# Optimization experiments

Measured on AMD Instinct MI355X. Metric: run time of the kernel, lower is better.

Reference implementation:

```python
import jax, jax.numpy as jnp
import numpy as np
from jax import lax

DN = ('NCHW', 'OIHW', 'NCHW')

def _conv(x, k, stride):
    return lax.conv_general_dilated(x, k, (stride, stride), 'VALID', dimension_numbers=DN)

def setup_inputs() -> dict:
    key = jax.random.key(0)
    ks = jax.random.split(key, 20)
    B, E, A, D = 2048, 8, 6, 64 * 7 * 7  # batch, rm_states, actions, flat conv dim (3136)
    s = 0.05
    inp = {
        'state': jax.random.normal(ks[0], (B, 84, 84, 3), jnp.float32),
        'rm_state': jax.random.randint(ks[1], (B,), 0, E, jnp.int64),
        # conv encoder params
        'k1': jax.random.normal(ks[2], (32, 3, 8, 8), jnp.float32) * s,
        'c1': jnp.zeros((32,), jnp.float32),
        'k2': jax.random.normal(ks[3], (64, 32, 4, 4), jnp.float32) * s,
        'c2': jnp.zeros((64,), jnp.float32),
        'k3': jax.random.normal(ks[4], (64, 64, 3, 3), jnp.float32) * s,
        'c3': jnp.zeros((64,), jnp.float32),
        # stacked per-rm-state expert MLP params (E experts)
        'W1': jax.random.normal(ks[5], (E, D, 64), jnp.float32) * s,
        'B1': jnp.zeros((E, 64), jnp.float32),
        'W2': jax.random.normal(ks[6], (E, 64, 64), jnp.float32) * s,
        'B2': jnp.zeros((E, 64), jnp.float32),
        'W3': jax.random.normal(ks[7], (E, 64, 64), jnp.float32) * s,
        'B3': jnp.zeros((E, 64), jnp.float32),
        'W4': jax.random.normal(ks[8], (E, 64, 64), jnp.float32) * s,
        'B4': jnp.zeros((E, 64), jnp.float32),
        'W5': jax.random.normal(ks[9], (E, 64, 64), jnp.float32) * s,
        'B5': jnp.zeros((E, 64), jnp.float32),
        'W6': jax.random.normal(ks[10], (E, 64, A), jnp.float32) * s,
        'B6': jnp.zeros((E, A), jnp.float32),
    }
    return inp

def reference(state, rm_state, k1, c1, k2, c2, k3, c3,
              W1, B1, W2, B2, W3, B3, W4, B4, W5, B5, W6, B6):
    # NHWC -> NCHW (matches torch's view-based channel-first rearrangement intent)
    x = jnp.transpose(state, (0, 3, 1, 2))
    x = jax.nn.relu(_conv(x, k1, 4) + c1[None, :, None, None])
    x = jax.nn.relu(_conv(x, k2, 2) + c2[None, :, None, None])
    x = jax.nn.relu(_conv(x, k3, 1) + c3[None, :, None, None])
    B = x.shape[0]
    flat = x.reshape(B, -1)                              # [B, 3136]
    # batched expert MLPs: compute all experts, then gather per-sample expert output
    h = jax.nn.relu(jnp.einsum('bd,edh->ebh', flat, W1) + B1[:, None, :])  # [E,B,64]
    for W, Bb in ((W2, B2), (W3, B3), (W4, B4), (W5, B5)):
        h = jax.nn.relu(jnp.einsum('ebh,ehk->ebk', h, W) + Bb[:, None, :])
    out = jnp.einsum('ebh,eha->eba', h, W6) + B6[:, None, :]               # [E,B,A]
    return out[rm_state, jnp.arange(B)]                  # [B, A]
```

## Files before the change

kernel.cpp:

```cpp
#include <hip/hip_runtime.h>

#define BATCH 2048

typedef unsigned short u16;
typedef __attribute__((ext_vector_type(8))) short bf16x8;
typedef __attribute__((ext_vector_type(4))) float f32x4;

static __device__ __forceinline__ float b2f(u16 h) {
  union { unsigned u; float f; } x; x.u = ((unsigned)h) << 16; return x.f;
}
static __device__ __forceinline__ u16 f2b(float f) {
  union { float f; unsigned u; } x; x.f = f;
  return (u16)((x.u + 0x7fffu + ((x.u >> 16) & 1u)) >> 16);
}
static __device__ __forceinline__ void split2(float v, u16& h, u16& l) {
  h = f2b(v); l = f2b(v - b2f(h));
}
static __device__ __forceinline__ bf16x8 ld8u(const u16* p, int idx) {
  union { bf16x8 v; ushort4 u[2]; } x;
  x.u[0] = *(const ushort4*)(p + idx);
  x.u[1] = *(const ushort4*)(p + idx + 4);
  return x.v;
}

__global__ void wsplit_kernel(const float* __restrict__ k1,
                              const float* __restrict__ k2,
                              const float* __restrict__ k3,
                              u16* __restrict__ W1d, u16* __restrict__ W2d,
                              u16* __restrict__ W3d)
{
  int id = blockIdx.x * 256 + threadIdx.x;
  float v; u16 *dh, *dl;
  if (id < 8192) {
    int ky = id >> 10, oc = (id >> 5) & 31, kk = id & 31;
    if (kk < 24) {
      int kx = kk / 3, c = kk - kx * 3;
      v = k1[oc * 192 + c * 64 + ky * 8 + kx];
    } else v = 0.f;
    dh = W1d + id; dl = W1d + 8192 + id;
  } else if (id < 40960) {
    int i = id - 8192;
    int pos = i >> 11, oc = (i >> 5) & 63, cc = i & 31;
    int ky = pos >> 2, kx = pos & 3;
    v = k2[oc * 512 + cc * 16 + ky * 4 + kx];
    dh = W2d + i; dl = W2d + 32768 + i;
  } else {
    int i = id - 40960;
    int j = i & 31, oc = (i >> 5) & 63, kc = (i >> 11) & 1, pos = i >> 12;
    int ky = pos / 3, kx = pos - ky * 3;
    v = k3[oc * 576 + (kc * 32 + j) * 9 + ky * 3 + kx];
    dh = W3d + i; dl = W3d + 36864 + i;
  }
  u16 h, l; split2(v, h, l); *dh = h; *dl = l;
}

__global__ __launch_bounds__(512, 4) void conv_fused_kernel(
    const float* __restrict__ state, const u16* __restrict__ W1d,
    const u16* __restrict__ W2d, const u16* __restrict__ W3d,
    const float* __restrict__ c1, const float* __restrict__ c2,
    const float* __restrict__ c3, float* __restrict__ a3)
{
  __shared__ __align__(16) u16 A1h[14400], A1l[14400];
  __shared__ __align__(16) u16 SHa[5832], SHb[5832];

  const int b = blockIdx.x, t = threadIdx.x;
  const int lane = t & 63, w = t >> 6, q = lane >> 4, n = lane & 15;

  for (int i = t; i < 792; i += 512) { SHa[5040 + i] = 0; SHb[5040 + i] = 0; }

  const int nT1 = (w < 2) ? 2 : 1;
  int pt1[2], ot1[2];
  if (w < 2) { pt1[0] = 0; ot1[0] = w; pt1[1] = 4; ot1[1] = w; }
  else       { pt1[0] = 1 + ((w - 2) >> 1); ot1[0] = (w - 2) & 1;
               pt1[1] = pt1[0]; ot1[1] = ot1[0]; }

  int aoff1[2];
  #pragma unroll
  for (int i = 0; i < 2; ++i) {
    int px = pt1[i] * 16 + n;
    int py = (px * 205) >> 12, pxx = px - py * 20;
    aoff1[i] = (py * 4) * 252 + pxx * 12 + q * 8;
  }
  float c1v[2];
  #pragma unroll
  for (int j = 0; j < 2; ++j) c1v[j] = c1[ot1[j] * 16 + n];
  const int ob1 = (ot1[0] * 16 + n) * 32 + q * 8;

  for (int by = 0; by < 5; ++by) {
    __syncthreads();
    const float4* sp = (const float4*)(state + (size_t)b * 21168 + by * 4032);
    #pragma unroll
    for (int pass = 0; pass < 3; ++pass) {
      int i = t + pass * 512;
      if (i < 1260) {
        float4 v = sp[i];
        u16 h0, l0, h1, l1, h2, l2, h3, l3;
        split2(v.x, h0, l0); split2(v.y, h1, l1);
        split2(v.z, h2, l2); split2(v.w, h3, l3);
        ushort4 hh; hh.x = h0; hh.y = h1; hh.z = h2; hh.w = h3;
        ushort4 ll; ll.x = l0; ll.y = l1; ll.z = l2; ll.w = l3;
        *(ushort4*)&SHa[i * 4] = hh;
        *(ushort4*)&SHb[i * 4] = ll;
      }
    }
    __syncthreads();

    f32x4 acc1[2] = {};
    bf16x8 bhc = *(const bf16x8*)(W1d + ob1);
    bf16x8 boc = *(const bf16x8*)(W1d + 8192 + ob1);
    for (int ky = 0; ky < 8; ++ky) {
      const int kyn = (ky < 7) ? ky + 1 : 7;
      bf16x8 bhn = *(const bf16x8*)(W1d + kyn * 1024 + ob1);
      bf16x8 bon = *(const bf16x8*)(W1d + 8192 + kyn * 1024 + ob1);
      #pragma unroll
      for (int i = 0; i < 2; ++i) if (i < nT1) {
        bf16x8 ah = ld8u(SHa, aoff1[i] + ky * 252);
        bf16x8 al = ld8u(SHb, aoff1[i] + ky * 252);
        acc1[i] = __builtin_amdgcn_mfma_f32_16x16x32_bf16(ah, bhc, acc1[i], 0, 0, 0);
        acc1[i] = __builtin_amdgcn_mfma_f32_16x16x32_bf16(ah, boc, acc1[i], 0, 0, 0);
        acc1[i] = __builtin_amdgcn_mfma_f32_16x16x32_bf16(al, bhc, acc1[i], 0, 0, 0);
      }
      bhc = bhn; boc = bon;
    }
    #pragma unroll
    for (int i = 0; i < 2; ++i) if (i < nT1) {
      int oc = ot1[i] * 16 + n;
      #pragma unroll
      for (int r = 0; r < 4; ++r) {
        int px = by * 80 + pt1[i] * 16 + q * 4 + r;
        float v = fmaxf(acc1[i][r] + c1v[i], 0.f);
        u16 h, l; split2(v, h, l);
        A1h[px * 36 + oc] = h; A1l[px * 36 + oc] = l;
      }
    }
  }
  __syncthreads();

  {
    const int ot2 = w & 3, pg2 = (w >> 2) * 3;
    int aoff2[3];
    #pragma unroll
    for (int i = 0; i < 3; ++i) {
      int px = (pg2 + i) * 16 + n; if (px > 80) px = 80;
      int py = (px * 7282) >> 16, pxx = px - py * 9;
      aoff2[i] = 2 * (py * 20 + pxx) * 36 + q * 8;
    }
    const float c2v = c2[ot2 * 16 + n];
    const int ob2 = (ot2 * 16 + n) * 32 + q * 8;

    f32x4 acc2[3] = {};
    bf16x8 bhc = *(const bf16x8*)(W2d + ob2);
    bf16x8 boc = *(const bf16x8*)(W2d + 32768 + ob2);
    for (int pos = 0; pos < 16; ++pos) {
      const int posn = (pos < 15) ? pos + 1 : 15;
      bf16x8 bhn = *(const bf16x8*)(W2d + posn * 2048 + ob2);
      bf16x8 bon = *(const bf16x8*)(W2d + 32768 + posn * 2048 + ob2);
      const int o = ((pos >> 2) * 20 + (pos & 3)) * 36;
      #pragma unroll
      for (int i = 0; i < 3; ++i) {
        bf16x8 ah = ld8u(A1h, aoff2[i] + o);
        bf16x8 al = ld8u(A1l, aoff2[i] + o);
        acc2[i] = __builtin_amdgcn_mfma_f32_16x16x32_bf16(ah, bhc, acc2[i], 0, 0, 0);
        acc2[i] = __builtin_amdgcn_mfma_f32_16x16x32_bf16(ah, boc, acc2[i], 0, 0, 0);
        acc2[i] = __builtin_amdgcn_mfma_f32_16x16x32_bf16(al, bhc, acc2[i], 0, 0, 0);
      }
      bhc = bhn; boc = bon;
    }
    #pragma unroll
    for (int i = 0; i < 3; ++i) {
      int oc = ot2 * 16 + n;
      #pragma unroll
      for (int r = 0; r < 4; ++r) {
        int px = (pg2 + i) * 16 + q * 4 + r;
        if (px < 81) {
          float v = fmaxf(acc2[i][r] + c2v, 0.f);
          u16 h, l; split2(v, h, l);
          SHa[px * 72 + oc] = h; SHb[px * 72 + oc] = l;
        }
      }
    }
  }
  __syncthreads();

  {
    const int ot3 = w & 3, pg3 = (w >> 2) * 2;
    int aoff3[2];
    #pragma unroll
    for (int i = 0; i < 2; ++i) {
      int px = (pg3 + i) * 16 + n; if (px > 48) px = 48;
      int py = (px * 74) >> 9, pxx = px - py * 7;
      aoff3[i] = (py * 9 + pxx) * 72 + q * 8;
    }
    const float c3v = c3[ot3 * 16 + n];
    const int ob3 = (ot3 * 16 + n) * 32 + q * 8;

    f32x4 acc3[2] = {};
    bf16x8 bhc = *(const bf16x8*)(W3d + ob3);
    bf16x8 boc = *(const bf16x8*)(W3d + 36864 + ob3);
    for (int pk = 0; pk < 18; ++pk) {
      const int pkn = (pk < 17) ? pk + 1 : 17;
      bf16x8 bhn = *(const bf16x8*)(W3d + pkn * 2048 + ob3);
      bf16x8 bon = *(const bf16x8*)(W3d + 36864 + pkn * 2048 + ob3);
      const int pos = pk >> 1, kc = pk & 1;
      const int ky = pos / 3, kx = pos - ky * 3;
      const int o = (ky * 9 + kx) * 72 + kc * 32;
      #pragma unroll
      for (int i = 0; i < 2; ++i) {
        bf16x8 ah = *(const bf16x8*)&SHa[aoff3[i] + o];
        bf16x8 al = *(const bf16x8*)&SHb[aoff3[i] + o];
        acc3[i] = __builtin_amdgcn_mfma_f32_16x16x32_bf16(ah, bhc, acc3[i], 0, 0, 0);
        acc3[i] = __builtin_amdgcn_mfma_f32_16x16x32_bf16(ah, boc, acc3[i], 0, 0, 0);
        acc3[i] = __builtin_amdgcn_mfma_f32_16x16x32_bf16(al, bhc, acc3[i], 0, 0, 0);
      }
      bhc = bhn; boc = bon;
    }
    float* op = a3 + (size_t)b * 3136;
    #pragma unroll
    for (int i = 0; i < 2; ++i) {
      int oc = ot3 * 16 + n;
      #pragma unroll
      for (int r = 0; r < 4; ++r) {
        int px = (pg3 + i) * 16 + q * 4 + r;
        if (px < 49) op[oc * 49 + px] = fmaxf(acc3[i][r] + c3v, 0.f);
      }
    }
  }
}

__global__ void group_kernel(const void* __restrict__ rmv,
                             int* __restrict__ counts, int* __restrict__ idxb)
{
  __shared__ int isI32;
  const int t = threadIdx.x;
  if (t == 0) isI32 = 0;
  if (t < 8) counts[t] = 0;
  __syncthreads();
  unsigned long long v = ((const unsigned long long*)rmv)[t];
  if (v >= 8ull) isI32 = 1;
  __syncthreads();
  const int i32 = isI32;
  for (int b = t; b < BATCH; b += 1024) {
    int e = i32 ? ((const int*)rmv)[b] : (int)((const long long*)rmv)[b];
    int pos = atomicAdd(&counts[e], 1);
    idxb[e * BATCH + pos] = b;
  }
}

__global__ __launch_bounds__(256) void gemm1_grp_kernel(
    const float* __restrict__ a3, const int* __restrict__ counts,
    const int* __restrict__ idxb, const float* __restrict__ W1,
    float* __restrict__ H1)
{
  __shared__ __align__(16) float At[32 * 68];
  __shared__ __align__(16) float Bw[32 * 64];
  __shared__ int s_id[64];
  const int e  = blockIdx.x >> 5;
  const int tl = blockIdx.x & 31;
  const int ks = blockIdx.y;
  const int cnt = counts[e];
  const int n0 = tl * 64;
  if (n0 >= cnt) return;
  const int m = min(64, cnt - n0);
  const int t = threadIdx.x;
  if (t < 64) s_id[t] = idxb[e * BATCH + n0 + min(t, m - 1)];
  __syncthreads();

  const int tx = t & 15, ty = t >> 4;
  const int c0 = tx * 4, r0 = ty * 4;
  const float* W1e = W1 + (size_t)e * 3136 * 64;
  float acc[4][4] = {};
  const int kbase = ks * 448;

  for (int k0 = kbase; k0 < kbase + 448; k0 += 32) {
    __syncthreads();
    {
      int i = t;
      #pragma unroll
      for (int pass = 0; pass < 2; ++pass, i += 256) {
        int r = i >> 3, k4 = (i & 7) * 4;
        float4 v = *(const float4*)(a3 + (size_t)s_id[r] * 3136 + k0 + k4);
        At[(k4 + 0) * 68 + r] = v.x; At[(k4 + 1) * 68 + r] = v.y;
        At[(k4 + 2) * 68 + r] = v.z; At[(k4 + 3) * 68 + r] = v.w;
      }
      int i2 = t;
      #pragma unroll
      for (int pass = 0; pass < 2; ++pass, i2 += 256) {
        int kk = i2 >> 4, h4 = (i2 & 15) * 4;
        *(float4*)&Bw[kk * 64 + h4] = *(const float4*)&W1e[(size_t)(k0 + kk) * 64 + h4];
      }
    }
    __syncthreads();
    #pragma unroll
    for (int kk = 0; kk < 32; ++kk) {
      float4 a = *(const float4*)&At[kk * 68 + r0];
      float4 bb = *(const float4*)&Bw[kk * 64 + c0];
      float av[4] = {a.x, a.y, a.z, a.w}, bv[4] = {bb.x, bb.y, bb.z, bb.w};
      #pragma unroll
      for (int ii = 0; ii < 4; ++ii)
        #pragma unroll
        for (int j = 0; j < 4; ++j)
          acc[ii][j] += av[ii] * bv[j];
    }
  }

  #pragma unroll
  for (int ii = 0; ii < 4; ++ii) {
    if (r0 + ii < m) {
      int s = s_id[r0 + ii];
      #pragma unroll
      for (int j = 0; j < 4; ++j)
        atomicAdd(&H1[(size_t)s * 64 + c0 + j], acc[ii][j]);
    }
  }
}

__global__ __launch_bounds__(256) void tail_grp_kernel(
    const float* __restrict__ H1, const int* __restrict__ counts,
    const int* __restrict__ idxb, const float* __restrict__ B1,
    const float* __restrict__ W2, const float* __restrict__ B2,
    const float* __restrict__ W3, const float* __restrict__ B3,
    const float* __restrict__ W4, const float* __restrict__ B4,
    const float* __restrict__ W5, const float* __restrict__ B5,
    const float* __restrict__ W6, const float* __restrict__ B6,
    float* __restrict__ out)
{
  __shared__ __align__(16) float Wl[4096];
  __shared__ float bl[64];
  __shared__ float W6l[384];
  __shared__ float B6l[8];
  __shared__ __align__(16) float Ht0[64 * 68];
  __shared__ __align__(16) float Ht1[64 * 68];
  __shared__ int s_id[64];

  const int e  = blockIdx.x >> 5;
  const int tl = blockIdx.x & 31;
  const int cnt = counts[e];
  const int n0 = tl * 64;
  if (n0 >= cnt) return;
  const int m = min(64, cnt - n0);
  const int t = threadIdx.x;
  if (t < 64) s_id[t] = idxb[e * BATCH + n0 + min(t, m - 1)];
  for (int i = t; i < 384; i += 256) W6l[i] = W6[e * 384 + i];
  if (t < 6)   B6l[t] = B6[e * 6 + t];
  __syncthreads();

  #pragma unroll
  for (int p = 0; p < 16; ++p) {
    int i = t + p * 256;
    int c = i & 63, r = i >> 6;
    Ht0[c * 68 + r] = fmaxf(H1[(size_t)s_id[r] * 64 + c] + B1[e * 64 + c], 0.f);
  }

  const int tx = t & 15, ty = t >> 4;
  const int c0 = tx * 4, r0 = ty * 4;
  const float* Ws[4] = {W2, W3, W4, W5};
  const float* Bs[4] = {B2, B3, B4, B5};
  float* Hc = Ht0; float* Hn = Ht1;

  for (int L = 0; L < 4; ++L) {
    __syncthreads();
    const float* We = Ws[L] + (size_t)e * 4096;
    for (int i = t; i < 1024; i += 256)
      *(float4*)&Wl[i * 4] = *(const float4*)&We[i * 4];
    if (t < 64) bl[t] = Bs[L][e * 64 + t];
    __syncthreads();

    float acc[4][4] = {};
    #pragma unroll 4
    for (int kk = 0; kk < 64; ++kk) {
      float4 a = *(const float4*)&Hc[kk * 68 + r0];
      float4 bb = *(const float4*)&Wl[kk * 64 + c0];
      float av[4] = {a.x, a.y, a.z, a.w}, bv[4] = {bb.x, bb.y, bb.z, bb.w};
      #pragma unroll
      for (int ii = 0; ii < 4; ++ii)
        #pragma unroll
        for (int j = 0; j < 4; ++j)
          acc[ii][j] += av[ii] * bv[j];
    }
    __syncthreads();
    #pragma unroll
    for (int j = 0; j < 4; ++j) {
      float bias = bl[c0 + j];
      #pragma unroll
      for (int ii = 0; ii < 4; ++ii)
        Hn[(c0 + j) * 68 + r0 + ii] = fmaxf(acc[ii][j] + bias, 0.f);
    }
    float* tmp = Hc; Hc = Hn; Hn = tmp;
  }
  __syncthreads();

  const int r = t & 63, aa = t >> 6;
  float s0v = 0.f, s1v = 0.f;
  for (int k = 0; k < 64; ++k) {
    float h = Hc[k * 68 + r];
    s0v += h * W6l[k * 6 + aa];
    s1v += h * W6l[k * 6 + ((aa < 2) ? aa + 4 : aa)];
  }
  if (r < m) {
    int s = s_id[r];
    out[s * 6 + aa] = s0v + B6l[aa];
    if (aa < 2) out[s * 6 + aa + 4] = s1v + B6l[aa + 4];
  }
}

extern "C" void kernel_launch(void* const* d_in, const int* in_sizes, int n_in,
                              void* d_out, int out_size, void* d_ws, size_t ws_size,
                              hipStream_t stream) {
  const float* state = (const float*)d_in[0];
  const void*  rm    = d_in[1];
  const float* k1 = (const float*)d_in[2];
  const float* c1 = (const float*)d_in[3];
  const float* k2 = (const float*)d_in[4];
  const float* c2 = (const float*)d_in[5];
  const float* k3 = (const float*)d_in[6];
  const float* c3 = (const float*)d_in[7];
  const float* W1 = (const float*)d_in[8];
  const float* B1 = (const float*)d_in[9];
  const float* W2 = (const float*)d_in[10];
  const float* B2 = (const float*)d_in[11];
  const float* W3 = (const float*)d_in[12];
  const float* B3 = (const float*)d_in[13];
  const float* W4 = (const float*)d_in[14];
  const float* B4 = (const float*)d_in[15];
  const float* W5 = (const float*)d_in[16];
  const float* B5 = (const float*)d_in[17];
  const float* W6 = (const float*)d_in[18];
  const float* B6 = (const float*)d_in[19];

  char* ws = (char*)d_ws;
  float* a3   = (float*)(ws);
  float* H1   = (float*)(ws + 25690112);
  int* counts = (int*)  (ws + 26214400);
  int* idxb   = (int*)  (ws + 26214432);
  u16* W1d    = (u16*)  (ws + 26280064);
  u16* W2d    = (u16*)  (ws + 26312832);
  u16* W3d    = (u16*)  (ws + 26443904);

  wsplit_kernel<<<304, 256, 0, stream>>>(k1, k2, k3, W1d, W2d, W3d);
  hipMemsetAsync(H1, 0, BATCH * 64 * sizeof(float), stream);
  group_kernel<<<1, 1024, 0, stream>>>(rm, counts, idxb);

  conv_fused_kernel<<<2048, 512, 0, stream>>>(state, W1d, W2d, W3d,
                                              c1, c2, c3, a3);

  gemm1_grp_kernel<<<dim3(256, 7), 256, 0, stream>>>(a3, counts, idxb, W1, H1);
  tail_grp_kernel<<<256, 256, 0, stream>>>(H1, counts, idxb, B1,
                                           W2, B2, W3, B3, W4, B4, W5, B5,
                                           W6, B6, (float*)d_out);
}
```

Before: 489.1 us.

## Fuse first expert GEMM into tail MLP kernel using split-bf16 MFMA

Conv output is now stored as hi/lo bf16 pairs, and W1 is pre-split into a tiled bf16 layout. The separate fp32 FMA GEMM1 kernel, which used a K-split with atomics into H1, is replaced by an MFMA-based three-term split-bf16 GEMM inside a single fused MLP kernel that then runs the remaining layers. This removes the H1 memset, the atomics, and one kernel launch. In exchange there is a per-call W1 split kernel and only 256 blocks, each running a 98-step K loop with no K-split, which may leave the GPU underutilized.

```diff
diff --git a/kernel.cpp b/kernel.cpp
--- a/kernel.cpp
+++ b/kernel.cpp
@@ -54,11 +54,25 @@
   u16 h, l; split2(v, h, l); *dh = h; *dl = l;
 }
 
+__global__ void w1split_kernel(const float* __restrict__ W1,
+                               u16* __restrict__ W1s)
+{
+  int id = blockIdx.x * 256 + threadIdx.x;
+  int e = id / 200704;
+  int r2 = id - e * 200704;
+  int k = r2 >> 6, c = r2 & 63;
+  float v = W1[id];
+  u16 h, l; split2(v, h, l);
+  int d = e * 200704 + (k >> 5) * 2048 + c * 32 + (k & 31);
+  W1s[d] = h; W1s[1605632 + d] = l;
+}
+
 __global__ __launch_bounds__(512, 4) void conv_fused_kernel(
     const float* __restrict__ state, const u16* __restrict__ W1d,
     const u16* __restrict__ W2d, const u16* __restrict__ W3d,
     const float* __restrict__ c1, const float* __restrict__ c2,
-    const float* __restrict__ c3, float* __restrict__ a3)
+    const float* __restrict__ c3, u16* __restrict__ a3h,
+    u16* __restrict__ a3l)
 {
   __shared__ __align__(16) u16 A1h[14400], A1l[14400];
   __shared__ __align__(16) u16 SHa[5832], SHb[5832];
@@ -214,14 +228,19 @@
       }
       bhc = bhn; boc = bon;
     }
-    float* op = a3 + (size_t)b * 3136;
+    u16* oph = a3h + (size_t)b * 3136;
+    u16* opl = a3l + (size_t)b * 3136;
     #pragma unroll
     for (int i = 0; i < 2; ++i) {
       int oc = ot3 * 16 + n;
       #pragma unroll
       for (int r = 0; r < 4; ++r) {
         int px = (pg3 + i) * 16 + q * 4 + r;
-        if (px < 49) op[oc * 49 + px] = fmaxf(acc3[i][r] + c3v, 0.f);
+        if (px < 49) {
+          float v = fmaxf(acc3[i][r] + c3v, 0.f);
+          u16 h, l; split2(v, h, l);
+          oph[oc * 49 + px] = h; opl[oc * 49 + px] = l;
+        }
       }
     }
   }
@@ -230,10 +249,11 @@
 __global__ void group_kernel(const void* __restrict__ rmv,
                              int* __restrict__ counts, int* __restrict__ idxb)
 {
+  __shared__ int lcnt[8];
   __shared__ int isI32;
   const int t = threadIdx.x;
   if (t == 0) isI32 = 0;
-  if (t < 8) counts[t] = 0;
+  if (t < 8) lcnt[t] = 0;
   __syncthreads();
   unsigned long long v = ((const unsigned long long*)rmv)[t];
   if (v >= 8ull) isI32 = 1;
@@ -241,82 +261,17 @@
   const int i32 = isI32;
   for (int b = t; b < BATCH; b += 1024) {
     int e = i32 ? ((const int*)rmv)[b] : (int)((const long long*)rmv)[b];
-    int pos = atomicAdd(&counts[e], 1);
+    int pos = atomicAdd(&lcnt[e], 1);
     idxb[e * BATCH + pos] = b;
   }
-}
-
-__global__ __launch_bounds__(256) void gemm1_grp_kernel(
-    const float* __restrict__ a3, const int* __restrict__ counts,
-    const int* __restrict__ idxb, const float* __restrict__ W1,
-    float* __restrict__ H1)
-{
-  __shared__ __align__(16) float At[32 * 68];
-  __shared__ __align__(16) float Bw[32 * 64];
-  __shared__ int s_id[64];
-  const int e  = blockIdx.x >> 5;
-  const int tl = blockIdx.x & 31;
-  const int ks = blockIdx.y;
-  const int cnt = counts[e];
-  const int n0 = tl * 64;
-  if (n0 >= cnt) return;
-  const int m = min(64, cnt - n0);
-  const int t = threadIdx.x;
-  if (t < 64) s_id[t] = idxb[e * BATCH + n0 + min(t, m - 1)];
-  __syncthreads();
-
-  const int tx = t & 15, ty = t >> 4;
-  const int c0 = tx * 4, r0 = ty * 4;
-  const float* W1e = W1 + (size_t)e * 3136 * 64;
-  float acc[4][4] = {};
-  const int kbase = ks * 448;
-
-  for (int k0 = kbase; k0 < kbase + 448; k0 += 32) {
-    __syncthreads();
-    {
-      int i = t;
-      #pragma unroll
-      for (int pass = 0; pass < 2; ++pass, i += 256) {
-        int r = i >> 3, k4 = (i & 7) * 4;
-        float4 v = *(const float4*)(a3 + (size_t)s_id[r] * 3136 + k0 + k4);
-        At[(k4 + 0) * 68 + r] = v.x; At[(k4 + 1) * 68 + r] = v.y;
-        At[(k4 + 2) * 68 + r] = v.z; At[(k4 + 3) * 68 + r] = v.w;
-      }
-      int i2 = t;
-      #pragma unroll
-      for (int pass = 0; pass < 2; ++pass, i2 += 256) {
-        int kk = i2 >> 4, h4 = (i2 & 15) * 4;
-        *(float4*)&Bw[kk * 64 + h4] = *(const float4*)&W1e[(size_t)(k0 + kk) * 64 + h4];
-      }
-    }
-    __syncthreads();
-    #pragma unroll
-    for (int kk = 0; kk < 32; ++kk) {
-      float4 a = *(const float4*)&At[kk * 68 + r0];
-      float4 bb = *(const float4*)&Bw[kk * 64 + c0];
-      float av[4] = {a.x, a.y, a.z, a.w}, bv[4] = {bb.x, bb.y, bb.z, bb.w};
-      #pragma unroll
-      for (int ii = 0; ii < 4; ++ii)
-        #pragma unroll
-        for (int j = 0; j < 4; ++j)
-          acc[ii][j] += av[ii] * bv[j];
-    }
-  }
-
-  #pragma unroll
-  for (int ii = 0; ii < 4; ++ii) {
-    if (r0 + ii < m) {
-      int s = s_id[r0 + ii];
-      #pragma unroll
-      for (int j = 0; j < 4; ++j)
-        atomicAdd(&H1[(size_t)s * 64 + c0 + j], acc[ii][j]);
-    }
-  }
-}
-
-__global__ __launch_bounds__(256) void tail_grp_kernel(
-    const float* __restrict__ H1, const int* __restrict__ counts,
-    const int* __restrict__ idxb, const float* __restrict__ B1,
+  __syncthreads();
+  if (t < 8) counts[t] = lcnt[t];
+}
+
+__global__ __launch_bounds__(512, 2) void mlp_kernel(
+    const u16* __restrict__ a3h, const u16* __restrict__ a3l,
+    const int* __restrict__ counts, const int* __restrict__ idxb,
+    const u16* __restrict__ W1s, const float* __restrict__ B1,
     const float* __restrict__ W2, const float* __restrict__ B2,
     const float* __restrict__ W3, const float* __restrict__ B3,
     const float* __restrict__ W4, const float* __restrict__ B4,
@@ -324,6 +279,7 @@
     const float* __restrict__ W6, const float* __restrict__ B6,
     float* __restrict__ out)
 {
+  __shared__ __align__(16) u16 Ah[2][2304], Al[2][2304];
   __shared__ __align__(16) float Wl[4096];
   __shared__ float bl[64];
   __shared__ float W6l[384];
@@ -339,20 +295,73 @@
   if (n0 >= cnt) return;
   const int m = min(64, cnt - n0);
   const int t = threadIdx.x;
-  if (t < 64) s_id[t] = idxb[e * BATCH + n0 + min(t, m - 1)];
-  for (int i = t; i < 384; i += 256) W6l[i] = W6[e * 384 + i];
+  if (t < 64)  s_id[t] = idxb[e * BATCH + n0 + min(t, m - 1)];
+  if (t < 384) W6l[t] = W6[e * 384 + t];
   if (t < 6)   B6l[t] = B6[e * 6 + t];
   __syncthreads();
 
-  #pragma unroll
-  for (int p = 0; p < 16; ++p) {
-    int i = t + p * 256;
-    int c = i & 63, r = i >> 6;
-    Ht0[c * 68 + r] = fmaxf(H1[(size_t)s_id[r] * 64 + c] + B1[e * 64 + c], 0.f);
+  const int lane = t & 63, w = t >> 6, q = lane >> 4, n = lane & 15;
+  const int mh = w >> 2, nt = w & 3;
+  const u16* Wb = W1s + (size_t)e * 200704;
+
+  const int sr = t >> 3, sub = t & 7, kp = sub & 3;
+  const u16* srcp = (sub < 4) ? a3h : a3l;
+  const size_t srow = (size_t)s_id[sr] * 3136;
+  const int aro = mh * 32 + n;
+  const int obase = (nt * 16 + n) * 32 + q * 8;
+
+  f32x4 acc0 = {}, acc1 = {};
+  {
+    ushort4 v0 = *(const ushort4*)(srcp + srow + kp * 8);
+    ushort4 v1 = *(const ushort4*)(srcp + srow + kp * 8 + 4);
+    u16* dst = (sub < 4) ? Ah[0] : Al[0];
+    *(ushort4*)&dst[sr * 36 + kp * 8]     = v0;
+    *(ushort4*)&dst[sr * 36 + kp * 8 + 4] = v1;
+  }
+  bf16x8 bhc = *(const bf16x8*)(Wb + obase);
+  bf16x8 boc = *(const bf16x8*)(Wb + 1605632 + obase);
+  __syncthreads();
+
+  for (int ch = 0; ch < 98; ++ch) {
+    const int cur = ch & 1;
+    if (ch < 97) {
+      const int k0n = (ch + 1) * 32;
+      ushort4 v0 = *(const ushort4*)(srcp + srow + k0n + kp * 8);
+      ushort4 v1 = *(const ushort4*)(srcp + srow + k0n + kp * 8 + 4);
+      u16* dst = (sub < 4) ? Ah[cur ^ 1] : Al[cur ^ 1];
+      *(ushort4*)&dst[sr * 36 + kp * 8]     = v0;
+      *(ushort4*)&dst[sr * 36 + kp * 8 + 4] = v1;
+    }
+    const int chn = (ch < 97) ? ch + 1 : 97;
+    bf16x8 bhn = *(const bf16x8*)(Wb + chn * 2048 + obase);
+    bf16x8 bon = *(const bf16x8*)(Wb + 1605632 + chn * 2048 + obase);
+
+    bf16x8 a0h = ld8u(Ah[cur], aro * 36 + q * 8);
+    bf16x8 a0l = ld8u(Al[cur], aro * 36 + q * 8);
+    bf16x8 a1h = ld8u(Ah[cur], (aro + 16) * 36 + q * 8);
+    bf16x8 a1l = ld8u(Al[cur], (aro + 16) * 36 + q * 8);
+    acc0 = __builtin_amdgcn_mfma_f32_16x16x32_bf16(a0h, bhc, acc0, 0, 0, 0);
+    acc0 = __builtin_amdgcn_mfma_f32_16x16x32_bf16(a0h, boc, acc0, 0, 0, 0);
+    acc0 = __builtin_amdgcn_mfma_f32_16x16x32_bf16(a0l, bhc, acc0, 0, 0, 0);
+    acc1 = __builtin_amdgcn_mfma_f32_16x16x32_bf16(a1h, bhc, acc1, 0, 0, 0);
+    acc1 = __builtin_amdgcn_mfma_f32_16x16x32_bf16(a1h, boc, acc1, 0, 0, 0);
+    acc1 = __builtin_amdgcn_mfma_f32_16x16x32_bf16(a1l, bhc, acc1, 0, 0, 0);
+    bhc = bhn; boc = bon;
+    __syncthreads();
+  }
+
+  {
+    const int c = nt * 16 + n;
+    const float b1v = B1[e * 64 + c];
+    #pragma unroll
+    for (int rr = 0; rr < 4; ++rr) {
+      Ht0[c * 68 + mh * 32 + q * 4 + rr]      = fmaxf(acc0[rr] + b1v, 0.f);
+      Ht0[c * 68 + mh * 32 + 16 + q * 4 + rr] = fmaxf(acc1[rr] + b1v, 0.f);
+    }
   }
 
   const int tx = t & 15, ty = t >> 4;
-  const int c0 = tx * 4, r0 = ty * 4;
+  const int c0 = tx * 4, r0 = ty * 2;
   const float* Ws[4] = {W2, W3, W4, W5};
   const float* Bs[4] = {B2, B3, B4, B5};
   float* Hc = Ht0; float* Hn = Ht1;
@@ -360,46 +369,40 @@
   for (int L = 0; L < 4; ++L) {
     __syncthreads();
     const float* We = Ws[L] + (size_t)e * 4096;
-    for (int i = t; i < 1024; i += 256)
+    for (int i = t; i < 1024; i += 512)
       *(float4*)&Wl[i * 4] = *(const float4*)&We[i * 4];
     if (t < 64) bl[t] = Bs[L][e * 64 + t];
     __syncthreads();
 
-    float acc[4][4] = {};
+    float acc[2][4] = {};
     #pragma unroll 4
     for (int kk = 0; kk < 64; ++kk) {
-      float4 a = *(const float4*)&Hc[kk * 68 + r0];
+      float a0 = Hc[kk * 68 + r0], a1 = Hc[kk * 68 + r0 + 1];
       float4 bb = *(const float4*)&Wl[kk * 64 + c0];
-      float av[4] = {a.x, a.y, a.z, a.w}, bv[4] = {bb.x, bb.y, bb.z, bb.w};
-      #pragma unroll
-      for (int ii = 0; ii < 4; ++ii)
-        #pragma unroll
-        for (int j = 0; j < 4; ++j)
-          acc[ii][j] += av[ii] * bv[j];
+      float bv[4] = {bb.x, bb.y, bb.z, bb.w};
+      #pragma unroll
+      for (int j = 0; j < 4; ++j) {
+        acc[0][j] += a0 * bv[j];
+        acc[1][j] += a1 * bv[j];
+      }
     }
     __syncthreads();
     #pragma unroll
     for (int j = 0; j < 4; ++j) {
       float bias = bl[c0 + j];
-      #pragma unroll
-      for (int ii = 0; ii < 4; ++ii)
-        Hn[(c0 + j) * 68 + r0 + ii] = fmaxf(acc[ii][j] + bias, 0.f);
+      Hn[(c0 + j) * 68 + r0]     = fmaxf(acc[0][j] + bias, 0.f);
+      Hn[(c0 + j) * 68 + r0 + 1] = fmaxf(acc[1][j] + bias, 0.f);
     }
     float* tmp = Hc; Hc = Hn; Hn = tmp;
   }
   __syncthreads();
 
   const int r = t & 63, aa = t >> 6;
-  float s0v = 0.f, s1v = 0.f;
-  for (int k = 0; k < 64; ++k) {
-    float h = Hc[k * 68 + r];
-    s0v += h * W6l[k * 6 + aa];
-    s1v += h * W6l[k * 6 + ((aa < 2) ? aa + 4 : aa)];
-  }
-  if (r < m) {
-    int s = s_id[r];
-    out[s * 6 + aa] = s0v + B6l[aa];
-    if (aa < 2) out[s * 6 + aa + 4] = s1v + B6l[aa + 4];
+  if (aa < 6) {
+    float s = 0.f;
+    for (int k = 0; k < 64; ++k)
+      s += Hc[k * 68 + r] * W6l[k * 6 + aa];
+    if (r < m) out[s_id[r] * 6 + aa] = s + B6l[aa];
   }
 }
 
@@ -428,23 +431,23 @@
   const float* B6 = (const float*)d_in[19];
 
   char* ws = (char*)d_ws;
-  float* a3   = (float*)(ws);
-  float* H1   = (float*)(ws + 25690112);
-  int* counts = (int*)  (ws + 26214400);
-  int* idxb   = (int*)  (ws + 26214432);
-  u16* W1d    = (u16*)  (ws + 26280064);
-  u16* W2d    = (u16*)  (ws + 26312832);
-  u16* W3d    = (u16*)  (ws + 26443904);
+  u16* a3h    = (u16*)(ws);
+  u16* a3l    = (u16*)(ws + 12845056);
+  int* counts = (int*)(ws + 25690112);
+  int* idxb   = (int*)(ws + 25690144);
+  u16* W1d    = (u16*)(ws + 25755680);
+  u16* W2d    = (u16*)(ws + 25788448);
+  u16* W3d    = (u16*)(ws + 25919520);
+  u16* W1s    = (u16*)(ws + 26066976);
 
   wsplit_kernel<<<304, 256, 0, stream>>>(k1, k2, k3, W1d, W2d, W3d);
-  hipMemsetAsync(H1, 0, BATCH * 64 * sizeof(float), stream);
+  w1split_kernel<<<6272, 256, 0, stream>>>(W1, W1s);
   group_kernel<<<1, 1024, 0, stream>>>(rm, counts, idxb);
 
   conv_fused_kernel<<<2048, 512, 0, stream>>>(state, W1d, W2d, W3d,
-                                              c1, c2, c3, a3);
-
-  gemm1_grp_kernel<<<dim3(256, 7), 256, 0, stream>>>(a3, counts, idxb, W1, H1);
-  tail_grp_kernel<<<256, 256, 0, stream>>>(H1, counts, idxb, B1,
-                                           W2, B2, W3, B3, W4, B4, W5, B5,
-                                           W6, B6, (float*)d_out);
-}
+                                              c1, c2, c3, a3h, a3l);
+
+  mlp_kernel<<<256, 512, 0, stream>>>(a3h, a3l, counts, idxb, W1s, B1,
+                                      W2, B2, W3, B3, W4, B4, W5, B5,
+                                      W6, B6, (float*)d_out);
+}
```

After: 471.8 us. -3.5%, faster.
